# Performance work log

Measured on AMD Instinct MI355X. Metric: run time of the kernel, lower is better.

The kernel has to match this reference:

```python
import jax, jax.numpy as jnp
import numpy as np

WS = 7            # window size
NW = 64           # windows per image ((56/7)^2)
SHIFT = 3         # shift size for the SW-MSA mask
HW = 56           # spatial patch grid


def _build_rel_index():
    coords = np.stack(np.meshgrid(np.arange(WS), np.arange(WS), indexing='ij'))  # [2,7,7]
    flat = coords.reshape(2, -1)                                                 # [2,49]
    rel = (flat[:, :, None] - flat[:, None, :]).transpose(1, 2, 0)               # [49,49,2]
    rel[:, :, 0] += WS - 1
    rel[:, :, 1] += WS - 1
    rel[:, :, 0] *= 2 * WS - 1
    return rel.sum(-1).astype(np.int32)                                          # [49,49]


def _build_shift_mask():
    img = np.zeros((HW, HW), dtype=np.float32)
    cnt = 0
    sl = (slice(0, -WS), slice(-WS, -SHIFT), slice(-SHIFT, None))
    for h in sl:
        for w in sl:
            img[h, w] = cnt
            cnt += 1
    # window partition -> [nW, 49]
    mw = img.reshape(HW // WS, WS, HW // WS, WS).transpose(0, 2, 1, 3).reshape(-1, WS * WS)
    am = mw[:, None, :] - mw[:, :, None]                                          # [nW,49,49]
    return np.where(am != 0, -100.0, 0.0).astype(np.float32)


def setup_inputs() -> dict:
    key = jax.random.key(0)
    ks = jax.random.split(key, 6)
    dim, heads, N = 128, 4, WS * WS
    B_ = 4096
    return {
        'x': jax.random.normal(ks[0], (B_, N, dim), dtype=jnp.float32),
        'qkv_w': jax.random.normal(ks[1], (dim, 3 * dim), dtype=jnp.float32) * 0.02,
        'qkv_b': jax.random.normal(ks[2], (3 * dim,), dtype=jnp.float32) * 0.02,
        'proj_w': jax.random.normal(ks[3], (dim, dim), dtype=jnp.float32) * 0.02,
        'proj_b': jax.random.normal(ks[4], (dim,), dtype=jnp.float32) * 0.02,
        'rel_bias_table': jax.random.normal(ks[5], ((2 * WS - 1) ** 2, heads), dtype=jnp.float32) * 0.02,
        'mask': jnp.asarray(_build_shift_mask()),
        'rel_index': jnp.asarray(_build_rel_index()),
    }


def reference(x, qkv_w, qkv_b, proj_w, proj_b, rel_bias_table, mask, rel_index):
    B_, N, C = x.shape
    heads = rel_bias_table.shape[1]
    hd = C // heads
    scale = hd ** -0.5
    # fused qkv projection: [B_, N, 3, H, hd]
    qkv = (x @ qkv_w + qkv_b).reshape(B_, N, 3, heads, hd)
    q, k, v = qkv[:, :, 0], qkv[:, :, 1], qkv[:, :, 2]      # [B_, N, H, hd]
    attn = jnp.einsum('bnhd,bmhd->bhnm', q, k) * scale       # [B_, H, N, N]
    # relative position bias gather: [N,N,H] -> [H,N,N]
    bias = rel_bias_table[rel_index].transpose(2, 0, 1)
    attn = attn + bias[None]
    # shifted-window mask: mask [nW, N, N]
    nW = mask.shape[0]
    attn = attn.reshape(B_ // nW, nW, heads, N, N) + mask[None, :, None]
    attn = attn.reshape(B_, heads, N, N)
    attn = jax.nn.softmax(attn, axis=-1)
    out = jnp.einsum('bhnm,bmhd->bnhd', attn, v).reshape(B_, N, C)
    return out @ proj_w + proj_b
```

## Files before the change

kernel.cpp:

```cpp
#include <hip/hip_runtime.h>
#include <hip/hip_bf16.h>

typedef __attribute__((ext_vector_type(8))) short bf16x8;
typedef __attribute__((ext_vector_type(4))) short s16x4;
typedef __attribute__((ext_vector_type(4))) float f32x4;

#define NTOK 49

#define XROW    136
#define RVB     8704
#define VBT_STR 68
#define VBT_SZ  2176
#define RQK     17408
#define QK_SZ   3920
#define SM_TOT  33088

__device__ __forceinline__ short f2b(float v) {
    __hip_bfloat16 b = __float2bfloat16(v);
    return *reinterpret_cast<short*>(&b);
}

__device__ __forceinline__ int rid_of(int t, int wh, int ww) {
    int i = t / 7;
    int j = t - 7 * i;
    int rh = (wh == 7) ? ((i < 4) ? 1 : 2) : 0;
    int rw = (ww == 7) ? ((j < 4) ? 1 : 2) : 0;
    return rh * 3 + rw;
}

__global__ void prep_kernel(const float* __restrict__ qkv_w,
                            const float* __restrict__ proj_w,
                            const float* __restrict__ rel_tab,
                            const int*   __restrict__ rel_idx,
                            short* __restrict__ wqkv_t,
                            short* __restrict__ wproj_t,
                            float* __restrict__ bmp2) {
    int i = blockIdx.x * 256 + threadIdx.x;
    if (i < 384 * 128) {
        int n = i >> 7, k = i & 127;
        wqkv_t[i] = f2b(qkv_w[k * 384 + n]);
        return;
    }
    int j = i - 384 * 128;
    if (j < 128 * 128) {
        int n = j >> 7, k = j & 127;
        wproj_t[j] = f2b(proj_w[k * 128 + n]);
        return;
    }
    int l = j - 128 * 128;
    if (l < 16 * NTOK * 64) {
        int wt  = l / (4 * NTOK * 64);
        int rem = l - wt * (4 * NTOK * 64);
        int h   = rem / (NTOK * 64);
        int rm2 = rem - h * (NTOK * 64);
        int q = rm2 >> 6, kk = rm2 & 63;
        float v;
        if (kk < NTOK) {
            v = rel_tab[rel_idx[q * NTOK + kk] * 4 + h];
            int wh = (wt & 1) ? 7 : 0, ww = (wt & 2) ? 7 : 0;
            if (rid_of(q, wh, ww) != rid_of(kk, wh, ww)) v -= 100.0f;
        } else {
            v = -1e30f;
        }
        bmp2[l] = v;
    }
}

__launch_bounds__(512, 4)
__global__ void swin_fused(const float* __restrict__ x,
                           const short* __restrict__ wqkv_t,
                           const float* __restrict__ qkv_b,
                           const short* __restrict__ wproj_t,
                           const float* __restrict__ proj_b,
                           const float* __restrict__ bmp2,
                           float* __restrict__ out) {
    __shared__ short sm[SM_TOT];

    const int b   = blockIdx.x;
    const int tid = threadIdx.x;
    const int wv  = tid >> 6;
    const int ln  = tid & 63;
    const int g   = ln >> 4;
    const int c   = ln & 15;
    const int h    = wv >> 1;
    const int half = wv & 1;

    short* vbt = sm + RVB + h * VBT_SZ;
    short* qbh = sm + RQK + h * QK_SZ;
    short* kbh = qbh + 1960;
    short* pbh = qbh;

    if (tid < 510) {
        *(s16x4*)&sm[NTOK * XROW + tid * 4] = (s16x4){0, 0, 0, 0};
    }
    for (int idx = tid; idx < 128 * 15; idx += 512) {
        int d = idx / 15, t = 49 + (idx - (idx / 15) * 15);
        sm[RVB + (d >> 5) * VBT_SZ + (d & 31) * VBT_STR + t] = 0;
    }
    {
        const f32x4* xp4 = (const f32x4*)(x + (size_t)b * 6272);
        f32x4 v0 = xp4[tid];
        f32x4 v1 = xp4[tid + 512];
        f32x4 v2 = xp4[tid + 1024];
        f32x4 v3;
        if (tid < 32) v3 = xp4[tid + 1536];
        #define XWR(IDX, V) { int row = (IDX) >> 5; int col = ((IDX) & 31) * 4; \
            s16x4 pk; pk[0]=f2b((V)[0]); pk[1]=f2b((V)[1]); pk[2]=f2b((V)[2]); pk[3]=f2b((V)[3]); \
            *(s16x4*)&sm[row * XROW + col] = pk; }
        XWR(tid, v0) XWR(tid + 512, v1) XWR(tid + 1024, v2)
        if (tid < 32) XWR(tid + 1536, v3)
        #undef XWR
    }
    __syncthreads();

    const int cq = 32 * h + 16 * half;

    {
        f32x4 accq[4], acck[4];
        #pragma unroll
        for (int nt = 0; nt < 4; ++nt) { accq[nt] = (f32x4){0.f,0.f,0.f,0.f}; acck[nt] = (f32x4){0.f,0.f,0.f,0.f}; }
        #pragma unroll
        for (int kt = 0; kt < 4; ++kt) {
            bf16x8 awq = *(const bf16x8*)&wqkv_t[(cq + c) * 128 + 32*kt + 8*g];
            bf16x8 awk = *(const bf16x8*)&wqkv_t[(128 + cq + c) * 128 + 32*kt + 8*g];
            bf16x8 xv[4];
            #pragma unroll
            for (int nt = 0; nt < 4; ++nt)
                xv[nt] = *(const bf16x8*)&sm[(16*nt + c) * XROW + 32*kt + 8*g];
            __builtin_amdgcn_s_setprio(1);
            #pragma unroll
            for (int nt = 0; nt < 4; ++nt) {
                accq[nt] = __builtin_amdgcn_mfma_f32_16x16x32_bf16(awq, xv[nt], accq[nt], 0, 0, 0);
                acck[nt] = __builtin_amdgcn_mfma_f32_16x16x32_bf16(awk, xv[nt], acck[nt], 0, 0, 0);
            }
            __builtin_amdgcn_s_setprio(0);
        }
        const float qsc = 0.17677669529663687f;
        f32x4 bq4 = *(const f32x4*)&qkv_b[cq + 4*g];
        f32x4 bk4 = *(const f32x4*)&qkv_b[128 + cq + 4*g];
        #pragma unroll
        for (int nt = 0; nt < 4; ++nt) {
            int tok = 16*nt + c;
            if (tok >= NTOK) continue;
            s16x4 pq, pk2;
            #pragma unroll
            for (int r = 0; r < 4; ++r) {
                pq[r]  = f2b((accq[nt][r] + bq4[r]) * qsc);
                pk2[r] = f2b(acck[nt][r] + bk4[r]);
            }
            *(s16x4*)&qbh[tok * 40 + 16*half + 4*g] = pq;
            *(s16x4*)&kbh[tok * 40 + 16*half + 4*g] = pk2;
        }
    }

    {
        f32x4 accv[4];
        #pragma unroll
        for (int nt = 0; nt < 4; ++nt) accv[nt] = (f32x4){0.f,0.f,0.f,0.f};
        #pragma unroll
        for (int kt = 0; kt < 4; ++kt) {
            bf16x8 awv = *(const bf16x8*)&wqkv_t[(256 + cq + c) * 128 + 32*kt + 8*g];
            bf16x8 xv[4];
            #pragma unroll
            for (int nt = 0; nt < 4; ++nt)
                xv[nt] = *(const bf16x8*)&sm[(16*nt + c) * XROW + 32*kt + 8*g];
            __builtin_amdgcn_s_setprio(1);
            #pragma unroll
            for (int nt = 0; nt < 4; ++nt)
                accv[nt] = __builtin_amdgcn_mfma_f32_16x16x32_bf16(awv, xv[nt], accv[nt], 0, 0, 0);
            __builtin_amdgcn_s_setprio(0);
        }
        f32x4 bv4 = *(const f32x4*)&qkv_b[256 + cq + 4*g];
        const int d0 = 16*half + 4*g;
        #pragma unroll
        for (int nt = 0; nt < 4; ++nt) {
            int tok = 16*nt + c;
            if (tok >= NTOK) continue;
            vbt[(d0+0) * VBT_STR + tok] = f2b(accv[nt][0] + bv4[0]);
            vbt[(d0+1) * VBT_STR + tok] = f2b(accv[nt][1] + bv4[1]);
            vbt[(d0+2) * VBT_STR + tok] = f2b(accv[nt][2] + bv4[2]);
            vbt[(d0+3) * VBT_STR + tok] = f2b(accv[nt][3] + bv4[3]);
        }
    }
    __syncthreads();

    const int ntq0 = 2 * half;
    const int wt = ((((b >> 3) & 7) == 7) ? 1 : 0) | (((b & 7) == 7) ? 2 : 0);
    const float* bbase = bmp2 + ((size_t)(wt * 4 + h) * NTOK) * 64;
    f32x4 bias0[4], bias1[4];
    {
        int q0c = 16*ntq0 + c;       if (q0c > 48) q0c = 48;
        int q1c = 16*(ntq0+1) + c;   if (q1c > 48) q1c = 48;
        const float* bp0 = bbase + (size_t)q0c * 64;
        const float* bp1 = bbase + (size_t)q1c * 64;
        #pragma unroll
        for (int mt = 0; mt < 4; ++mt) {
            bias0[mt] = *(const f32x4*)&bp0[16*mt + 4*g];
            bias1[mt] = *(const f32x4*)&bp1[16*mt + 4*g];
        }
    }
    f32x4 sA[4][2];
    {
        #pragma unroll
        for (int mt = 0; mt < 4; ++mt) { sA[mt][0] = (f32x4){0.f,0.f,0.f,0.f}; sA[mt][1] = (f32x4){0.f,0.f,0.f,0.f}; }
        bf16x8 ak[4];
        #pragma unroll
        for (int mt = 0; mt < 4; ++mt) {
            int kt2 = 16*mt + c; if (kt2 > 48) kt2 = 48;
            ak[mt] = *(const bf16x8*)&kbh[kt2 * 40 + 8*g];
        }
        __builtin_amdgcn_s_setprio(1);
        #pragma unroll
        for (int jj = 0; jj < 2; ++jj) {
            int qt = 16*(ntq0+jj) + c; if (qt > 48) qt = 48;
            bf16x8 bq = *(const bf16x8*)&qbh[qt * 40 + 8*g];
            #pragma unroll
            for (int mt = 0; mt < 4; ++mt)
                sA[mt][jj] = __builtin_amdgcn_mfma_f32_16x16x32_bf16(ak[mt], bq, sA[mt][jj], 0, 0, 0);
        }
        __builtin_amdgcn_s_setprio(0);
    }
    __syncthreads();

    {
        #pragma unroll
        for (int jj = 0; jj < 2; ++jj) {
            int qtok = 16*(ntq0+jj) + c;
            const f32x4* bias = jj ? bias1 : bias0;
            float e[16];
            float mx = -1e30f;
            #pragma unroll
            for (int mt = 0; mt < 4; ++mt) {
                #pragma unroll
                for (int r = 0; r < 4; ++r) {
                    float v = sA[mt][jj][r] + bias[mt][r];
                    e[4*mt+r] = v;
                    mx = fmaxf(mx, v);
                }
            }
            mx = fmaxf(mx, __shfl_xor(mx, 16, 64));
            mx = fmaxf(mx, __shfl_xor(mx, 32, 64));
            float s = 0.f;
            #pragma unroll
            for (int ii = 0; ii < 16; ++ii) { float ev = __expf(e[ii] - mx); e[ii] = ev; s += ev; }
            s += __shfl_xor(s, 16, 64);
            s += __shfl_xor(s, 32, 64);
            float rs = 1.0f / s;
            if (qtok < NTOK) {
                #pragma unroll
                for (int mt = 0; mt < 4; ++mt) {
                    s16x4 pk;
                    pk[0] = f2b(e[4*mt+0] * rs);
                    pk[1] = f2b(e[4*mt+1] * rs);
                    pk[2] = f2b(e[4*mt+2] * rs);
                    pk[3] = f2b(e[4*mt+3] * rs);
                    *(s16x4*)&pbh[qtok * 72 + 16*mt + 4*g] = pk;
                }
            }
        }

        f32x4 o[2][2];
        o[0][0]=(f32x4){0.f,0.f,0.f,0.f}; o[0][1]=(f32x4){0.f,0.f,0.f,0.f};
        o[1][0]=(f32x4){0.f,0.f,0.f,0.f}; o[1][1]=(f32x4){0.f,0.f,0.f,0.f};
        __builtin_amdgcn_s_setprio(1);
        #pragma unroll
        for (int kt = 0; kt < 2; ++kt) {
            bf16x8 av[2];
            #pragma unroll
            for (int mt = 0; mt < 2; ++mt)
                av[mt] = *(const bf16x8*)&vbt[(16*mt + c) * VBT_STR + 32*kt + 8*g];
            #pragma unroll
            for (int jj = 0; jj < 2; ++jj) {
                int qt = 16*(ntq0+jj) + c; if (qt > 48) qt = 48;
                bf16x8 bp2 = *(const bf16x8*)&pbh[qt * 72 + 32*kt + 8*g];
                #pragma unroll
                for (int mt = 0; mt < 2; ++mt)
                    o[mt][jj] = __builtin_amdgcn_mfma_f32_16x16x32_bf16(av[mt], bp2, o[mt][jj], 0, 0, 0);
            }
        }
        __builtin_amdgcn_s_setprio(0);
        #pragma unroll
        for (int jj = 0; jj < 2; ++jj) {
            int qtok = 16*(ntq0+jj) + c;
            if (qtok >= NTOK) continue;
            #pragma unroll
            for (int mt = 0; mt < 2; ++mt) {
                s16x4 pko;
                pko[0] = f2b(o[mt][jj][0]); pko[1] = f2b(o[mt][jj][1]);
                pko[2] = f2b(o[mt][jj][2]); pko[3] = f2b(o[mt][jj][3]);
                *(s16x4*)&pbh[qtok * 72 + 16*mt + 4*g] = pko;
            }
        }
    }
    __syncthreads();

    {
        const int chb = 16 * wv;
        f32x4 po[4];
        #pragma unroll
        for (int j = 0; j < 4; ++j) po[j] = (f32x4){0.f,0.f,0.f,0.f};
        #pragma unroll
        for (int kt = 0; kt < 4; ++kt) {
            bf16x8 aw = *(const bf16x8*)&wproj_t[(chb + c) * 128 + 32*kt + 8*g];
            const short* ob_kt = sm + RQK + kt * QK_SZ;
            __builtin_amdgcn_s_setprio(1);
            #pragma unroll
            for (int j = 0; j < 4; ++j) {
                int qt = 16*j + c; if (qt > 48) qt = 48;
                bf16x8 bo = *(const bf16x8*)&ob_kt[qt * 72 + 8*g];
                po[j] = __builtin_amdgcn_mfma_f32_16x16x32_bf16(aw, bo, po[j], 0, 0, 0);
            }
            __builtin_amdgcn_s_setprio(0);
        }
        f32x4 pb4 = *(const f32x4*)&proj_b[chb + 4*g];
        float* op = out + (size_t)b * 6272;
        #pragma unroll
        for (int j = 0; j < 4; ++j) {
            int qtok = 16*j + c;
            if (qtok >= NTOK) continue;
            f32x4 w;
            w[0] = po[j][0] + pb4[0]; w[1] = po[j][1] + pb4[1];
            w[2] = po[j][2] + pb4[2]; w[3] = po[j][3] + pb4[3];
            *(f32x4*)&op[qtok * 128 + chb + 4*g] = w;
        }
    }
}

extern "C" void kernel_launch(void* const* d_in, const int* in_sizes, int n_in,
                              void* d_out, int out_size, void* d_ws, size_t ws_size,
                              hipStream_t stream) {
    const float* x       = (const float*)d_in[0];
    const float* qkv_w   = (const float*)d_in[1];
    const float* qkv_b   = (const float*)d_in[2];
    const float* proj_w  = (const float*)d_in[3];
    const float* proj_b  = (const float*)d_in[4];
    const float* rel_tab = (const float*)d_in[5];
    const int*   rel_idx = (const int*)d_in[7];

    char* ws = (char*)d_ws;
    short* wqkv_t  = (short*)ws;
    short* wproj_t = (short*)(ws + 98304);
    float* bmp2    = (float*)(ws + 98304 + 32768);

    int total = 384*128 + 128*128 + 16*NTOK*64;
    prep_kernel<<<(total + 255) / 256, 256, 0, stream>>>(qkv_w, proj_w, rel_tab, rel_idx,
                                                         wqkv_t, wproj_t, bmp2);

    int B_ = in_sizes[0] / (NTOK * 128);
    swin_fused<<<B_, 512, 0, stream>>>(x, wqkv_t, qkv_b, wproj_t, proj_b, bmp2,
                                       (float*)d_out);
}
```

Before: 132.4 us.

## Use exp2 softmax, defer normalization, prefetch weights, drop setprio, move barrier

Folds log2(e) into the q scale and the precomputed bias/mask table so the softmax can use exp2f. Normalization is deferred: unnormalized probabilities go to shared memory and the reciprocal sum is applied to the PV output, which moves the cross-lane sum shuffles off the store path. Weight fragments for Q/K, V and the projection are loaded into registers ahead of use (Q/K before the first barrier), and the bias loads are hoisted ahead of the post-QKV barrier. All s_setprio hints are removed. This raises register pressure under the 4-block launch bound.

```diff
diff --git a/kernel.cpp b/kernel.cpp
--- a/kernel.cpp
+++ b/kernel.cpp
@@ -49,6 +49,7 @@
     }
     int l = j - 128 * 128;
     if (l < 16 * NTOK * 64) {
+        const float LOG2E = 1.4426950408889634f;
         int wt  = l / (4 * NTOK * 64);
         int rem = l - wt * (4 * NTOK * 64);
         int h   = rem / (NTOK * 64);
@@ -56,9 +57,9 @@
         int q = rm2 >> 6, kk = rm2 & 63;
         float v;
         if (kk < NTOK) {
-            v = rel_tab[rel_idx[q * NTOK + kk] * 4 + h];
+            v = rel_tab[rel_idx[q * NTOK + kk] * 4 + h] * LOG2E;
             int wh = (wt & 1) ? 7 : 0, ww = (wt & 2) ? 7 : 0;
-            if (rid_of(q, wh, ww) != rid_of(kk, wh, ww)) v -= 100.0f;
+            if (rid_of(q, wh, ww) != rid_of(kk, wh, ww)) v -= 100.0f * LOG2E;
         } else {
             v = -1e30f;
         }
@@ -89,6 +90,8 @@
     short* qbh = sm + RQK + h * QK_SZ;
     short* kbh = qbh + 1960;
     short* pbh = qbh;
+
+    const int cq = 32 * h + 16 * half;
 
     if (tid < 510) {
         *(s16x4*)&sm[NTOK * XROW + tid * 4] = (s16x4){0, 0, 0, 0};
@@ -111,31 +114,36 @@
         if (tid < 32) XWR(tid + 1536, v3)
         #undef XWR
     }
+    bf16x8 wqr[4], wkr[4];
+    #pragma unroll
+    for (int kt = 0; kt < 4; ++kt) {
+        wqr[kt] = *(const bf16x8*)&wqkv_t[(cq + c) * 128 + 32*kt + 8*g];
+        wkr[kt] = *(const bf16x8*)&wqkv_t[(128 + cq + c) * 128 + 32*kt + 8*g];
+    }
     __syncthreads();
 
-    const int cq = 32 * h + 16 * half;
-
+    bf16x8 wvr[4];
     {
         f32x4 accq[4], acck[4];
         #pragma unroll
         for (int nt = 0; nt < 4; ++nt) { accq[nt] = (f32x4){0.f,0.f,0.f,0.f}; acck[nt] = (f32x4){0.f,0.f,0.f,0.f}; }
         #pragma unroll
         for (int kt = 0; kt < 4; ++kt) {
-            bf16x8 awq = *(const bf16x8*)&wqkv_t[(cq + c) * 128 + 32*kt + 8*g];
-            bf16x8 awk = *(const bf16x8*)&wqkv_t[(128 + cq + c) * 128 + 32*kt + 8*g];
             bf16x8 xv[4];
             #pragma unroll
             for (int nt = 0; nt < 4; ++nt)
                 xv[nt] = *(const bf16x8*)&sm[(16*nt + c) * XROW + 32*kt + 8*g];
-            __builtin_amdgcn_s_setprio(1);
             #pragma unroll
             for (int nt = 0; nt < 4; ++nt) {
-                accq[nt] = __builtin_amdgcn_mfma_f32_16x16x32_bf16(awq, xv[nt], accq[nt], 0, 0, 0);
-                acck[nt] = __builtin_amdgcn_mfma_f32_16x16x32_bf16(awk, xv[nt], acck[nt], 0, 0, 0);
-            }
-            __builtin_amdgcn_s_setprio(0);
-        }
-        const float qsc = 0.17677669529663687f;
+                accq[nt] = __builtin_amdgcn_mfma_f32_16x16x32_bf16(wqr[kt], xv[nt], accq[nt], 0, 0, 0);
+                acck[nt] = __builtin_amdgcn_mfma_f32_16x16x32_bf16(wkr[kt], xv[nt], acck[nt], 0, 0, 0);
+            }
+        }
+        #pragma unroll
+        for (int kt = 0; kt < 4; ++kt)
+            wvr[kt] = *(const bf16x8*)&wqkv_t[(256 + cq + c) * 128 + 32*kt + 8*g];
+
+        const float qsc = 0.17677669529663687f * 1.4426950408889634f;
         f32x4 bq4 = *(const f32x4*)&qkv_b[cq + 4*g];
         f32x4 bk4 = *(const f32x4*)&qkv_b[128 + cq + 4*g];
         #pragma unroll
@@ -159,16 +167,13 @@
         for (int nt = 0; nt < 4; ++nt) accv[nt] = (f32x4){0.f,0.f,0.f,0.f};
         #pragma unroll
         for (int kt = 0; kt < 4; ++kt) {
-            bf16x8 awv = *(const bf16x8*)&wqkv_t[(256 + cq + c) * 128 + 32*kt + 8*g];
             bf16x8 xv[4];
             #pragma unroll
             for (int nt = 0; nt < 4; ++nt)
                 xv[nt] = *(const bf16x8*)&sm[(16*nt + c) * XROW + 32*kt + 8*g];
-            __builtin_amdgcn_s_setprio(1);
             #pragma unroll
             for (int nt = 0; nt < 4; ++nt)
-                accv[nt] = __builtin_amdgcn_mfma_f32_16x16x32_bf16(awv, xv[nt], accv[nt], 0, 0, 0);
-            __builtin_amdgcn_s_setprio(0);
+                accv[nt] = __builtin_amdgcn_mfma_f32_16x16x32_bf16(wvr[kt], xv[nt], accv[nt], 0, 0, 0);
         }
         f32x4 bv4 = *(const f32x4*)&qkv_b[256 + cq + 4*g];
         const int d0 = 16*half + 4*g;
@@ -182,7 +187,6 @@
             vbt[(d0+3) * VBT_STR + tok] = f2b(accv[nt][3] + bv4[3]);
         }
     }
-    __syncthreads();
 
     const int ntq0 = 2 * half;
     const int wt = ((((b >> 3) & 7) == 7) ? 1 : 0) | (((b & 7) == 7) ? 2 : 0);
@@ -199,6 +203,8 @@
             bias1[mt] = *(const f32x4*)&bp1[16*mt + 4*g];
         }
     }
+    __syncthreads();
+
     f32x4 sA[4][2];
     {
         #pragma unroll
@@ -209,7 +215,6 @@
             int kt2 = 16*mt + c; if (kt2 > 48) kt2 = 48;
             ak[mt] = *(const bf16x8*)&kbh[kt2 * 40 + 8*g];
         }
-        __builtin_amdgcn_s_setprio(1);
         #pragma unroll
         for (int jj = 0; jj < 2; ++jj) {
             int qt = 16*(ntq0+jj) + c; if (qt > 48) qt = 48;
@@ -218,11 +223,11 @@
             for (int mt = 0; mt < 4; ++mt)
                 sA[mt][jj] = __builtin_amdgcn_mfma_f32_16x16x32_bf16(ak[mt], bq, sA[mt][jj], 0, 0, 0);
         }
-        __builtin_amdgcn_s_setprio(0);
     }
     __syncthreads();
 
     {
+        float rs01[2];
         #pragma unroll
         for (int jj = 0; jj < 2; ++jj) {
             int qtok = 16*(ntq0+jj) + c;
@@ -242,27 +247,26 @@
             mx = fmaxf(mx, __shfl_xor(mx, 32, 64));
             float s = 0.f;
             #pragma unroll
-            for (int ii = 0; ii < 16; ++ii) { float ev = __expf(e[ii] - mx); e[ii] = ev; s += ev; }
-            s += __shfl_xor(s, 16, 64);
-            s += __shfl_xor(s, 32, 64);
-            float rs = 1.0f / s;
+            for (int ii = 0; ii < 16; ++ii) { float ev = exp2f(e[ii] - mx); e[ii] = ev; s += ev; }
             if (qtok < NTOK) {
                 #pragma unroll
                 for (int mt = 0; mt < 4; ++mt) {
                     s16x4 pk;
-                    pk[0] = f2b(e[4*mt+0] * rs);
-                    pk[1] = f2b(e[4*mt+1] * rs);
-                    pk[2] = f2b(e[4*mt+2] * rs);
-                    pk[3] = f2b(e[4*mt+3] * rs);
+                    pk[0] = f2b(e[4*mt+0]);
+                    pk[1] = f2b(e[4*mt+1]);
+                    pk[2] = f2b(e[4*mt+2]);
+                    pk[3] = f2b(e[4*mt+3]);
                     *(s16x4*)&pbh[qtok * 72 + 16*mt + 4*g] = pk;
                 }
             }
+            s += __shfl_xor(s, 16, 64);
+            s += __shfl_xor(s, 32, 64);
+            rs01[jj] = 1.0f / s;
         }
 
         f32x4 o[2][2];
         o[0][0]=(f32x4){0.f,0.f,0.f,0.f}; o[0][1]=(f32x4){0.f,0.f,0.f,0.f};
         o[1][0]=(f32x4){0.f,0.f,0.f,0.f}; o[1][1]=(f32x4){0.f,0.f,0.f,0.f};
-        __builtin_amdgcn_s_setprio(1);
         #pragma unroll
         for (int kt = 0; kt < 2; ++kt) {
             bf16x8 av[2];
@@ -278,16 +282,16 @@
                     o[mt][jj] = __builtin_amdgcn_mfma_f32_16x16x32_bf16(av[mt], bp2, o[mt][jj], 0, 0, 0);
             }
         }
-        __builtin_amdgcn_s_setprio(0);
         #pragma unroll
         for (int jj = 0; jj < 2; ++jj) {
             int qtok = 16*(ntq0+jj) + c;
             if (qtok >= NTOK) continue;
+            float rs = rs01[jj];
             #pragma unroll
             for (int mt = 0; mt < 2; ++mt) {
                 s16x4 pko;
-                pko[0] = f2b(o[mt][jj][0]); pko[1] = f2b(o[mt][jj][1]);
-                pko[2] = f2b(o[mt][jj][2]); pko[3] = f2b(o[mt][jj][3]);
+                pko[0] = f2b(o[mt][jj][0] * rs); pko[1] = f2b(o[mt][jj][1] * rs);
+                pko[2] = f2b(o[mt][jj][2] * rs); pko[3] = f2b(o[mt][jj][3] * rs);
                 *(s16x4*)&pbh[qtok * 72 + 16*mt + 4*g] = pko;
             }
         }
@@ -296,23 +300,24 @@
 
     {
         const int chb = 16 * wv;
+        bf16x8 awr[4];
+        #pragma unroll
+        for (int kt = 0; kt < 4; ++kt)
+            awr[kt] = *(const bf16x8*)&wproj_t[(chb + c) * 128 + 32*kt + 8*g];
+        f32x4 pb4 = *(const f32x4*)&proj_b[chb + 4*g];
         f32x4 po[4];
         #pragma unroll
         for (int j = 0; j < 4; ++j) po[j] = (f32x4){0.f,0.f,0.f,0.f};
         #pragma unroll
         for (int kt = 0; kt < 4; ++kt) {
-            bf16x8 aw = *(const bf16x8*)&wproj_t[(chb + c) * 128 + 32*kt + 8*g];
             const short* ob_kt = sm + RQK + kt * QK_SZ;
-            __builtin_amdgcn_s_setprio(1);
             #pragma unroll
             for (int j = 0; j < 4; ++j) {
                 int qt = 16*j + c; if (qt > 48) qt = 48;
                 bf16x8 bo = *(const bf16x8*)&ob_kt[qt * 72 + 8*g];
-                po[j] = __builtin_amdgcn_mfma_f32_16x16x32_bf16(aw, bo, po[j], 0, 0, 0);
-            }
-            __builtin_amdgcn_s_setprio(0);
-        }
-        f32x4 pb4 = *(const f32x4*)&proj_b[chb + 4*g];
+                po[j] = __builtin_amdgcn_mfma_f32_16x16x32_bf16(awr[kt], bo, po[j], 0, 0, 0);
+            }
+        }
         float* op = out + (size_t)b * 6272;
         #pragma unroll
         for (int j = 0; j < 4; ++j) {
```

Result: faster. 129.4 us (-2.3%).
